# Performance work log

Hardware: AMD Instinct MI355X
Metric: run time of the kernel (lower is better)

Reference implementation:

```python
import jax, jax.numpy as jnp
import numpy as np

EPS = 1e-5

def layer_norm(x, w, b):
    mu = jnp.mean(x, axis=-1, keepdims=True)
    var = jnp.mean(jnp.square(x - mu), axis=-1, keepdims=True)
    return (x - mu) * jax.lax.rsqrt(var + EPS) * w + b

def setup_inputs() -> dict:
    key = jax.random.key(0)
    ks = jax.random.split(key, 8)
    B, T, C = 8, 512, 768
    s = 1.0 / np.sqrt(C)
    s4 = 1.0 / np.sqrt(4 * C)
    return {
        "x": jax.random.normal(ks[0], (B, T, C), dtype=jnp.float32),
        "ln1_w": jnp.ones((C,), jnp.float32),
        "ln1_b": jnp.zeros((C,), jnp.float32),
        "Wr": jax.random.normal(ks[1], (C, C), dtype=jnp.float32) * s,
        "Wk": jax.random.normal(ks[2], (C, C), dtype=jnp.float32) * s,
        "Wv": jax.random.normal(ks[3], (C, C), dtype=jnp.float32) * s,
        "time_mix_w": jnp.ones((C,), jnp.float32),  # torch init: torch.ones(n_embd)
        "Wrouter": jax.random.normal(ks[4], (C, C), dtype=jnp.float32) * s,
        "ln2_w": jnp.ones((C,), jnp.float32),
        "ln2_b": jnp.zeros((C,), jnp.float32),
        "Wck": jax.random.normal(ks[5], (4 * C, C), dtype=jnp.float32) * s,
        "Wcv": jax.random.normal(ks[6], (C, 4 * C), dtype=jnp.float32) * s4,
    }

def reference(x, ln1_w, ln1_b, Wr, Wk, Wv, time_mix_w, Wrouter, ln2_w, ln2_b, Wck, Wcv):
    B, T, C = x.shape
    xx = layer_norm(x, ln1_w, ln1_b)
    r = xx @ Wr.T
    k = xx @ Wk.T
    v = xx @ Wv.T
    w = -jnp.exp(time_mix_w)                        # (C,) negative per-channel decay rate
    idx = jnp.arange(T)
    diff = jnp.clip(idx[:, None] - idx[None, :], 0).astype(x.dtype)  # (T,T) t-j clamped at 0
    causal = jnp.tril(jnp.ones((T, T), x.dtype))
    decay = jnp.exp(w[:, None, None] * diff[None]) * causal          # (C,T,T)
    kv = k * v                                                       # (B,T,C)
    # wkv[b,t,c] = sum_j decay[c,t,j] * kv[b,j,c]
    wkv = jnp.einsum('ctj,bjc->btc', decay, kv)
    routed_wkv = wkv * jax.nn.sigmoid(xx @ Wrouter.T)
    x = x + r * routed_wkv
    xx2 = layer_norm(x, ln2_w, ln2_b)
    k_cm = jnp.square(jax.nn.relu(xx2 @ Wck.T))                      # (B,T,4C)
    return x + k_cm @ Wcv.T
```

## Files before the change

### kernel.cpp

```cpp
#include <hip/hip_runtime.h>
#include <hip/hip_bf16.h>

typedef __bf16 bf16_t;
typedef __bf16 bf16x8 __attribute__((ext_vector_type(8)));
typedef __bf16 bf16x4 __attribute__((ext_vector_type(4)));
typedef float  f32x4  __attribute__((ext_vector_type(4)));

#define LN_EPS 1e-5f


typedef __attribute__((address_space(1))) void gvoid_t;
typedef __attribute__((address_space(3))) void lvoid_t;
__device__ __forceinline__ void glds16(const void* g, void* l) {
    __builtin_amdgcn_global_load_lds((gvoid_t*)g, (lvoid_t*)l, 16, 0, 0);
}

__global__ __launch_bounds__(256) void k_cvt4(const float* __restrict__ s0,
                                              const float* __restrict__ s1,
                                              const float* __restrict__ s2,
                                              const float* __restrict__ s3,
                                              bf16_t* __restrict__ dst, int n4) {
    const float* s = (blockIdx.y == 0) ? s0 : (blockIdx.y == 1) ? s1 : (blockIdx.y == 2) ? s2 : s3;
    bf16_t* d = dst + (size_t)blockIdx.y * ((size_t)n4 * 4);
    int i = blockIdx.x * 256 + threadIdx.x;
    if (i < n4) {
        float4 v = ((const float4*)s)[i];
        bf16x4 o;
        o.x = (bf16_t)v.x; o.y = (bf16_t)v.y; o.z = (bf16_t)v.z; o.w = (bf16_t)v.w;
        ((bf16x4*)d)[i] = o;
    }
}

__global__ __launch_bounds__(256) void k_cvt2(const float* __restrict__ s0,
                                              const float* __restrict__ s1,
                                              bf16_t* __restrict__ dst, int n4) {
    const float* s = (blockIdx.y == 0) ? s0 : s1;
    bf16_t* d = dst + (size_t)blockIdx.y * ((size_t)n4 * 4);
    int i = blockIdx.x * 256 + threadIdx.x;
    if (i < n4) {
        float4 v = ((const float4*)s)[i];
        bf16x4 o;
        o.x = (bf16_t)v.x; o.y = (bf16_t)v.y; o.z = (bf16_t)v.z; o.w = (bf16_t)v.w;
        ((bf16x4*)d)[i] = o;
    }
}

__global__ __launch_bounds__(256) void k_ln(const float* __restrict__ x,
                                            const float* __restrict__ w,
                                            const float* __restrict__ b,
                                            bf16_t* __restrict__ out, int C) {
    int row = blockIdx.x;
    const float* xr = x + (long)row * C;
    int tid = threadIdx.x;
    float s = 0.f, s2 = 0.f;
    for (int i = tid; i < C; i += 256) { float v = xr[i]; s += v; s2 += v * v; }
    for (int m = 32; m; m >>= 1) { s += __shfl_xor(s, m, 64); s2 += __shfl_xor(s2, m, 64); }
    __shared__ float red[8];
    int wv = tid >> 6;
    if ((tid & 63) == 0) { red[wv] = s; red[4 + wv] = s2; }
    __syncthreads();
    float ts  = red[0] + red[1] + red[2] + red[3];
    float ts2 = red[4] + red[5] + red[6] + red[7];
    float mu  = ts / C;
    float var = ts2 / C - mu * mu;
    float rstd = rsqrtf(var + LN_EPS);
    bf16_t* orow = out + (long)row * C;
    for (int i = tid; i < C; i += 256)
        orow[i] = (bf16_t)((xr[i] - mu) * rstd * w[i] + b[i]);
}

template <int EPI>
__global__ __launch_bounds__(512, 2) void k_gemm_bt(const bf16_t* __restrict__ A,
                                                    const bf16_t* __restrict__ Bw,
                                                    void* __restrict__ Cout,
                                                    int N, int Ktot, int nbn, int nks) {
    constexpr int TBUF = 256 * 32;
    __shared__ __align__(16) bf16_t As[4][256][32];
    __shared__ __align__(16) bf16_t Bs[4][256][32];
    const int tid  = threadIdx.x;
    const int lane = tid & 63, wid = tid >> 6;
    const int wm = (wid >> 2) * 128, wn = (wid & 3) * 64;

    int bid = blockIdx.x;
    int swz = (bid & 7) * 24 + (bid >> 3);
    int per_m = nbn * nks;
    int bm  = swz / per_m;
    int rem = swz % per_m;
    int ks  = rem / nbn;
    int bn  = rem % nbn;

    const int fr = lane & 15;
    const int swcol = (((lane >> 4) ^ (lane >> 2)) & 3) * 8;

    f32x4 acc[8][4];
#pragma unroll
    for (int i = 0; i < 8; i++)
#pragma unroll
        for (int j = 0; j < 4; j++) acc[i][j] = (f32x4){0.f, 0.f, 0.f, 0.f};

    const int srow = wid * 32 + (lane >> 2);
    const int scol = (((lane & 3) ^ (lane >> 4)) & 3) * 8;
    const bf16_t* Ag = A  + (size_t)(bm * 256 + srow) * Ktot + (size_t)ks * 768 + scol;
    const bf16_t* Bg = Bw + (size_t)(bn * 256 + srow) * Ktot + (size_t)ks * 768 + scol;
    const size_t Kt16 = (size_t)16 * Ktot;
    bf16_t* lA = &As[0][wid * 32][0];
    bf16_t* lB = &Bs[0][wid * 32][0];

#define STAGE(buf, kt)                                            \
    do {                                                          \
        const bf16_t* a0 = Ag + (size_t)(kt) * 32;                \
        const bf16_t* b0 = Bg + (size_t)(kt) * 32;                \
        glds16(a0,        lA + (buf) * TBUF);                     \
        glds16(a0 + Kt16, lA + (buf) * TBUF + 16 * 32);           \
        glds16(b0,        lB + (buf) * TBUF);                     \
        glds16(b0 + Kt16, lB + (buf) * TBUF + 16 * 32);           \
    } while (0)

#define COMPUTE(buf)                                                                         \
    do {                                                                                     \
        const bf16_t* pA = &As[0][0][0] + (buf) * TBUF + (wm + fr) * 32 + swcol;             \
        const bf16_t* pB = &Bs[0][0][0] + (buf) * TBUF + (wn + fr) * 32 + swcol;             \
        bf16x8 af[8], bfr[4];                                                                \
        _Pragma("unroll")                                                                    \
        for (int mi = 0; mi < 8; mi++) af[mi] = *(const bf16x8*)(pA + mi * 512);             \
        _Pragma("unroll")                                                                    \
        for (int ni = 0; ni < 4; ni++) bfr[ni] = *(const bf16x8*)(pB + ni * 512);            \
        __builtin_amdgcn_s_setprio(1);                                                       \
        _Pragma("unroll")                                                                    \
        for (int mi = 0; mi < 8; mi++)                                                       \
            _Pragma("unroll")                                                                \
            for (int ni = 0; ni < 4; ni++)                                                   \
                acc[mi][ni] = __builtin_amdgcn_mfma_f32_16x16x32_bf16(af[mi], bfr[ni], acc[mi][ni], 0, 0, 0); \
        __builtin_amdgcn_s_setprio(0);                                                       \
    } while (0)

    STAGE(0, 0);
    STAGE(1, 1);
    for (int s = 0; s < 22; ++s) {
        asm volatile("s_waitcnt vmcnt(4)" ::: "memory");
        __builtin_amdgcn_s_barrier();
        __builtin_amdgcn_sched_barrier(0);
        STAGE((s + 2) & 3, s + 2);
        COMPUTE(s & 3);
    }
    asm volatile("s_waitcnt vmcnt(4)" ::: "memory");
    __builtin_amdgcn_s_barrier();
    __builtin_amdgcn_sched_barrier(0);
    COMPUTE(2);
    asm volatile("s_waitcnt vmcnt(0)" ::: "memory");
    __builtin_amdgcn_s_barrier();
    __builtin_amdgcn_sched_barrier(0);
    COMPUTE(3);

#undef STAGE
#undef COMPUTE

    const int row0 = bm * 256 + wm, col0 = bn * 256 + wn;
#pragma unroll
    for (int mi = 0; mi < 8; mi++) {
#pragma unroll
        for (int ni = 0; ni < 4; ni++) {
            int row = row0 + mi * 16 + (lane >> 4) * 4;
            int col = col0 + ni * 16 + (lane & 15);
#pragma unroll
            for (int r = 0; r < 4; r++) {
                float val = acc[mi][ni][r];
                size_t off = (size_t)(row + r) * N + col;
                if (EPI == 0) {
                    ((bf16_t*)Cout)[off] = (bf16_t)val;
                } else if (EPI == 1) {
                    float t = fmaxf(val, 0.f);
                    ((bf16_t*)Cout)[off] = (bf16_t)(t * t);
                } else {
                    atomicAdd(&((float*)Cout)[off], val);
                }
            }
        }
    }
}

__global__ __launch_bounds__(256) void k_scan_local(const bf16_t* __restrict__ y4,
                                                    const float* __restrict__ tmw,
                                                    float* __restrict__ wkvl,
                                                    float* __restrict__ states) {
    int idx = blockIdx.x * 256 + threadIdx.x;
    int c   = idx % 768;
    int rem = idx / 768;
    int ch  = rem & 15;
    int b   = rem >> 4;
    float d = expf(-expf(tmw[c]));
    const bf16_t* base = y4 + ((size_t)(b * 512 + ch * 32)) * 3072 + c;
    float*        wout = wkvl + ((size_t)(b * 512 + ch * 32)) * 768 + c;
    float s = 0.f;
#pragma unroll 4
    for (int i = 0; i < 32; i++) {
        float kk = (float)base[(size_t)i * 3072 + 768];
        float vv = (float)base[(size_t)i * 3072 + 1536];
        s = s * d + kk * vv;
        wout[(size_t)i * 768] = s;
    }
    states[idx] = s;
}

__global__ __launch_bounds__(256) void k_scan_carry(const float* __restrict__ states,
                                                    const float* __restrict__ tmw,
                                                    float* __restrict__ carries) {
    int idx = blockIdx.x * 256 + threadIdx.x;
    int c = idx % 768, b = idx / 768;
    float dL = expf(-expf(tmw[c]) * 32.f);
    float s = 0.f;
    for (int ch = 0; ch < 16; ch++) {
        size_t o = ((size_t)(b * 16 + ch)) * 768 + c;
        carries[o] = s;
        s = s * dL + states[o];
    }
}

__global__ __launch_bounds__(256) void k_mix_ln(const bf16_t* __restrict__ y4,
                                                const float* __restrict__ wkvl,
                                                const float* __restrict__ carries,
                                                const float* __restrict__ tmw,
                                                const float* __restrict__ x,
                                                const float* __restrict__ w2,
                                                const float* __restrict__ b2,
                                                float* __restrict__ out,
                                                bf16_t* __restrict__ xx2) {
    int bt = blockIdx.x;
    int t = bt & 511, b = bt >> 9;
    int tid = threadIdx.x;
    const bf16_t* yrow = y4 + (size_t)bt * 3072;
    const float*  wl   = wkvl + (size_t)bt * 768;
    const float*  cr   = carries + ((size_t)(b * 16) + (t >> 5)) * 768;
    const float*  xr   = x + (size_t)bt * 768;
    float tn = (float)((t & 31) + 1);

    float vals[3];
    float s = 0.f, s2 = 0.f;
#pragma unroll
    for (int j = 0; j < 3; j++) {
        int c = tid + j * 256;
        float rr = (float)yrow[c];
        float gg = (float)yrow[c + 2304];
        float wk = wl[c] + cr[c] * expf(-expf(tmw[c]) * tn);
        float sig = 1.f / (1.f + expf(-gg));
        float o = fmaf(rr, wk * sig, xr[c]);
        vals[j] = o; s += o; s2 += o * o;
    }
    for (int m = 32; m; m >>= 1) { s += __shfl_xor(s, m, 64); s2 += __shfl_xor(s2, m, 64); }
    __shared__ float red[8];
    int wv = tid >> 6;
    if ((tid & 63) == 0) { red[wv] = s; red[4 + wv] = s2; }
    __syncthreads();
    float ts  = red[0] + red[1] + red[2] + red[3];
    float ts2 = red[4] + red[5] + red[6] + red[7];
    float mu  = ts * (1.f / 768.f);
    float var = ts2 * (1.f / 768.f) - mu * mu;
    float rstd = rsqrtf(var + LN_EPS);
    float* orow = out + (size_t)bt * 768;
    bf16_t* xo = xx2 + (size_t)bt * 768;
#pragma unroll
    for (int j = 0; j < 3; j++) {
        int c = tid + j * 256;
        orow[c] = vals[j];
        xo[c] = (bf16_t)((vals[j] - mu) * rstd * w2[c] + b2[c]);
    }
}

extern "C" void kernel_launch(void* const* d_in, const int* in_sizes, int n_in,
                              void* d_out, int out_size, void* d_ws, size_t ws_size,
                              hipStream_t stream) {
    const float* x    = (const float*)d_in[0];
    const float* ln1w = (const float*)d_in[1];
    const float* ln1b = (const float*)d_in[2];
    const float* Wr   = (const float*)d_in[3];
    const float* Wk   = (const float*)d_in[4];
    const float* Wv   = (const float*)d_in[5];
    const float* tmw  = (const float*)d_in[6];
    const float* Wrt  = (const float*)d_in[7];
    const float* ln2w = (const float*)d_in[8];
    const float* ln2b = (const float*)d_in[9];
    const float* Wck  = (const float*)d_in[10];
    const float* Wcv  = (const float*)d_in[11];
    float* out = (float*)d_out;
    char* ws = (char*)d_ws;

    bf16_t* xx     = (bf16_t*)(ws + 0);
    bf16_t* wcat   = (bf16_t*)(ws + 6291456);
    bf16_t* wckb   = (bf16_t*)(ws + 11010048);
    bf16_t* wcvb   = (bf16_t*)(ws + 15728640);
    bf16_t* y4     = (bf16_t*)(ws + 20447232);
    bf16_t* kcm    = (bf16_t*)(ws + 20447232);
    float*  wkvl   = (float*)(ws + 70778880);
    float*  states = (float*)(ws + 83361792);
    float*  carr   = (float*)(ws + 83755008);

    const int n768 = 768 * 768 / 4;
    const int nbig = 3072 * 768 / 4;
    k_cvt4<<<dim3(576, 4), dim3(256), 0, stream>>>(Wr, Wk, Wv, Wrt, wcat, n768);
    k_cvt2<<<dim3(2304, 2), dim3(256), 0, stream>>>(Wck, Wcv, wckb, nbig);

    k_ln<<<dim3(4096), dim3(256), 0, stream>>>(x, ln1w, ln1b, xx, 768);

    k_gemm_bt<0><<<dim3(192), dim3(512), 0, stream>>>(xx, wcat, (void*)y4, 3072, 768, 12, 1);

    k_scan_local<<<dim3(384), dim3(256), 0, stream>>>(y4, tmw, wkvl, states);
    k_scan_carry<<<dim3(24), dim3(256), 0, stream>>>(states, tmw, carr);
    k_mix_ln<<<dim3(4096), dim3(256), 0, stream>>>(y4, wkvl, carr, tmw, x, ln2w, ln2b, out, xx);

    k_gemm_bt<1><<<dim3(192), dim3(512), 0, stream>>>(xx, wckb, (void*)kcm, 3072, 768, 12, 1);

    k_gemm_bt<3><<<dim3(192), dim3(512), 0, stream>>>(kcm, wcvb, (void*)out, 768, 3072, 3, 4);
}
```

Before: 182.0 us.

## Shrink GEMM tiles to 64x128 with more blocks, vectorize scan over channel pairs

The bf16 GEMM switches from 256x256 tiles with 512 threads and 4-stage LDS buffering to 64x128 tiles with 256 threads and plain double buffering. Grid size grows from 192 to 1536 blocks, with a new XCD-aware block mapping, to fill all CUs. The local scan now handles two channels per thread using bf16x2 loads and float2 stores. The smaller tiles give less operand reuse per block and more global/L2 traffic, and the simpler pipeline relies on higher occupancy to hide load latency.

Result: no change. 179.7 us (-1.3%).

```diff
diff --git a/kernel.cpp b/kernel.cpp
--- a/kernel.cpp
+++ b/kernel.cpp
@@ -4,6 +4,7 @@
 typedef __bf16 bf16_t;
 typedef __bf16 bf16x8 __attribute__((ext_vector_type(8)));
 typedef __bf16 bf16x4 __attribute__((ext_vector_type(4)));
+typedef __bf16 bf16x2 __attribute__((ext_vector_type(2)));
 typedef float  f32x4  __attribute__((ext_vector_type(4)));
 
 #define LN_EPS 1e-5f
@@ -70,64 +71,63 @@
 }
 
 template <int EPI>
-__global__ __launch_bounds__(512, 2) void k_gemm_bt(const bf16_t* __restrict__ A,
+__global__ __launch_bounds__(256, 6) void k_gemm_bt(const bf16_t* __restrict__ A,
                                                     const bf16_t* __restrict__ Bw,
                                                     void* __restrict__ Cout,
                                                     int N, int Ktot, int nbn, int nks) {
-    constexpr int TBUF = 256 * 32;
-    __shared__ __align__(16) bf16_t As[4][256][32];
-    __shared__ __align__(16) bf16_t Bs[4][256][32];
+    constexpr int ABUF = 64 * 32;
+    constexpr int BBUF = 128 * 32;
+    __shared__ __align__(16) bf16_t As[2][64][32];
+    __shared__ __align__(16) bf16_t Bs[2][128][32];
     const int tid  = threadIdx.x;
     const int lane = tid & 63, wid = tid >> 6;
-    const int wm = (wid >> 2) * 128, wn = (wid & 3) * 64;
+    const int wm = (wid >> 1) * 32, wn = (wid & 1) * 64;
 
     int bid = blockIdx.x;
-    int swz = (bid & 7) * 24 + (bid >> 3);
-    int per_m = nbn * nks;
-    int bm  = swz / per_m;
-    int rem = swz % per_m;
-    int ks  = rem / nbn;
-    int bn  = rem % nbn;
+    int xcd = bid & 7, loc = bid >> 3;
+    int bm  = (xcd >> 1) * 16 + loc / 12;
+    int cix = (xcd & 1) * 12 + loc % 12;
+    int ks  = cix / nbn;
+    int bn  = cix % nbn;
 
     const int fr = lane & 15;
     const int swcol = (((lane >> 4) ^ (lane >> 2)) & 3) * 8;
 
-    f32x4 acc[8][4];
-#pragma unroll
-    for (int i = 0; i < 8; i++)
+    f32x4 acc[2][4];
+#pragma unroll
+    for (int i = 0; i < 2; i++)
 #pragma unroll
         for (int j = 0; j < 4; j++) acc[i][j] = (f32x4){0.f, 0.f, 0.f, 0.f};
 
-    const int srow = wid * 32 + (lane >> 2);
+    const int rsub = lane >> 2;
     const int scol = (((lane & 3) ^ (lane >> 4)) & 3) * 8;
-    const bf16_t* Ag = A  + (size_t)(bm * 256 + srow) * Ktot + (size_t)ks * 768 + scol;
-    const bf16_t* Bg = Bw + (size_t)(bn * 256 + srow) * Ktot + (size_t)ks * 768 + scol;
+    const bf16_t* Ag = A  + (size_t)(bm * 64  + wid * 16 + rsub) * Ktot + (size_t)ks * 768 + scol;
+    const bf16_t* Bg = Bw + (size_t)(bn * 128 + wid * 32 + rsub) * Ktot + (size_t)ks * 768 + scol;
     const size_t Kt16 = (size_t)16 * Ktot;
-    bf16_t* lA = &As[0][wid * 32][0];
+    bf16_t* lA = &As[0][wid * 16][0];
     bf16_t* lB = &Bs[0][wid * 32][0];
 
 #define STAGE(buf, kt)                                            \
     do {                                                          \
         const bf16_t* a0 = Ag + (size_t)(kt) * 32;                \
         const bf16_t* b0 = Bg + (size_t)(kt) * 32;                \
-        glds16(a0,        lA + (buf) * TBUF);                     \
-        glds16(a0 + Kt16, lA + (buf) * TBUF + 16 * 32);           \
-        glds16(b0,        lB + (buf) * TBUF);                     \
-        glds16(b0 + Kt16, lB + (buf) * TBUF + 16 * 32);           \
+        glds16(a0,        lA + (buf) * ABUF);                     \
+        glds16(b0,        lB + (buf) * BBUF);                     \
+        glds16(b0 + Kt16, lB + (buf) * BBUF + 16 * 32);           \
     } while (0)
 
 #define COMPUTE(buf)                                                                         \
     do {                                                                                     \
-        const bf16_t* pA = &As[0][0][0] + (buf) * TBUF + (wm + fr) * 32 + swcol;             \
-        const bf16_t* pB = &Bs[0][0][0] + (buf) * TBUF + (wn + fr) * 32 + swcol;             \
-        bf16x8 af[8], bfr[4];                                                                \
+        const bf16_t* pA = &As[0][0][0] + (buf) * ABUF + (wm + fr) * 32 + swcol;             \
+        const bf16_t* pB = &Bs[0][0][0] + (buf) * BBUF + (wn + fr) * 32 + swcol;             \
+        bf16x8 af[2], bfr[4];                                                                \
         _Pragma("unroll")                                                                    \
-        for (int mi = 0; mi < 8; mi++) af[mi] = *(const bf16x8*)(pA + mi * 512);             \
+        for (int mi = 0; mi < 2; mi++) af[mi] = *(const bf16x8*)(pA + mi * 512);             \
         _Pragma("unroll")                                                                    \
         for (int ni = 0; ni < 4; ni++) bfr[ni] = *(const bf16x8*)(pB + ni * 512);            \
         __builtin_amdgcn_s_setprio(1);                                                       \
         _Pragma("unroll")                                                                    \
-        for (int mi = 0; mi < 8; mi++)                                                       \
+        for (int mi = 0; mi < 2; mi++)                                                       \
             _Pragma("unroll")                                                                \
             for (int ni = 0; ni < 4; ni++)                                                   \
                 acc[mi][ni] = __builtin_amdgcn_mfma_f32_16x16x32_bf16(af[mi], bfr[ni], acc[mi][ni], 0, 0, 0); \
@@ -135,29 +135,22 @@
     } while (0)
 
     STAGE(0, 0);
-    STAGE(1, 1);
-    for (int s = 0; s < 22; ++s) {
-        asm volatile("s_waitcnt vmcnt(4)" ::: "memory");
-        __builtin_amdgcn_s_barrier();
-        __builtin_amdgcn_sched_barrier(0);
-        STAGE((s + 2) & 3, s + 2);
-        COMPUTE(s & 3);
-    }
-    asm volatile("s_waitcnt vmcnt(4)" ::: "memory");
-    __builtin_amdgcn_s_barrier();
-    __builtin_amdgcn_sched_barrier(0);
-    COMPUTE(2);
-    asm volatile("s_waitcnt vmcnt(0)" ::: "memory");
-    __builtin_amdgcn_s_barrier();
-    __builtin_amdgcn_sched_barrier(0);
-    COMPUTE(3);
+    __syncthreads();
+    int cur = 0;
+    for (int kt = 0; kt < 23; ++kt) {
+        STAGE(cur ^ 1, kt + 1);
+        COMPUTE(cur);
+        __syncthreads();
+        cur ^= 1;
+    }
+    COMPUTE(cur);
 
 #undef STAGE
 #undef COMPUTE
 
-    const int row0 = bm * 256 + wm, col0 = bn * 256 + wn;
-#pragma unroll
-    for (int mi = 0; mi < 8; mi++) {
+    const int row0 = bm * 64 + wm, col0 = bn * 128 + wn;
+#pragma unroll
+    for (int mi = 0; mi < 2; mi++) {
 #pragma unroll
         for (int ni = 0; ni < 4; ni++) {
             int row = row0 + mi * 16 + (lane >> 4) * 4;
@@ -184,22 +177,25 @@
                                                     float* __restrict__ wkvl,
                                                     float* __restrict__ states) {
     int idx = blockIdx.x * 256 + threadIdx.x;
-    int c   = idx % 768;
-    int rem = idx / 768;
+    int cp  = idx % 384;
+    int rem = idx / 384;
     int ch  = rem & 15;
     int b   = rem >> 4;
-    float d = expf(-expf(tmw[c]));
+    int c   = cp * 2;
+    float d0 = expf(-expf(tmw[c]));
+    float d1 = expf(-expf(tmw[c + 1]));
     const bf16_t* base = y4 + ((size_t)(b * 512 + ch * 32)) * 3072 + c;
     float*        wout = wkvl + ((size_t)(b * 512 + ch * 32)) * 768 + c;
-    float s = 0.f;
+    float s0 = 0.f, s1 = 0.f;
 #pragma unroll 4
     for (int i = 0; i < 32; i++) {
-        float kk = (float)base[(size_t)i * 3072 + 768];
-        float vv = (float)base[(size_t)i * 3072 + 1536];
-        s = s * d + kk * vv;
-        wout[(size_t)i * 768] = s;
-    }
-    states[idx] = s;
+        bf16x2 k2 = *(const bf16x2*)(base + (size_t)i * 3072 + 768);
+        bf16x2 v2 = *(const bf16x2*)(base + (size_t)i * 3072 + 1536);
+        s0 = s0 * d0 + (float)k2.x * (float)v2.x;
+        s1 = s1 * d1 + (float)k2.y * (float)v2.y;
+        *(float2*)(wout + (size_t)i * 768) = make_float2(s0, s1);
+    }
+    *(float2*)(states + ((size_t)(b * 16 + ch)) * 768 + c) = make_float2(s0, s1);
 }
 
 __global__ __launch_bounds__(256) void k_scan_carry(const float* __restrict__ states,
@@ -301,13 +297,13 @@
 
     k_ln<<<dim3(4096), dim3(256), 0, stream>>>(x, ln1w, ln1b, xx, 768);
 
-    k_gemm_bt<0><<<dim3(192), dim3(512), 0, stream>>>(xx, wcat, (void*)y4, 3072, 768, 12, 1);
-
-    k_scan_local<<<dim3(384), dim3(256), 0, stream>>>(y4, tmw, wkvl, states);
+    k_gemm_bt<0><<<dim3(1536), dim3(256), 0, stream>>>(xx, wcat, (void*)y4, 3072, 768, 24, 1);
+
+    k_scan_local<<<dim3(192), dim3(256), 0, stream>>>(y4, tmw, wkvl, states);
     k_scan_carry<<<dim3(24), dim3(256), 0, stream>>>(states, tmw, carr);
     k_mix_ln<<<dim3(4096), dim3(256), 0, stream>>>(y4, wkvl, carr, tmw, x, ln2w, ln2b, out, xx);
 
-    k_gemm_bt<1><<<dim3(192), dim3(512), 0, stream>>>(xx, wckb, (void*)kcm, 3072, 768, 12, 1);
-
-    k_gemm_bt<3><<<dim3(192), dim3(512), 0, stream>>>(kcm, wcvb, (void*)out, 768, 3072, 3, 4);
-}
+    k_gemm_bt<1><<<dim3(1536), dim3(256), 0, stream>>>(xx, wckb, (void*)kcm, 3072, 768, 24, 1);
+
+    k_gemm_bt<3><<<dim3(1536), dim3(256), 0, stream>>>(kcm, wcvb, (void*)out, 768, 3072, 6, 4);
+}
```
